# Kernel optimization log

Hardware: AMD Instinct MI355X
Metric: run time of the kernel (lower is better)

## Reference

```python
import jax, jax.numpy as jnp
import numpy as np

N_INPUT, N_QUBITS, N_LAYERS, N_CLASSES, BATCH = 64, 10, 6, 2, 16384


def _apply_1q(state, axis, m00, m01, m10, m11):
    # state: (B, 2,...,2) complex; axis is the tensor axis of the target wire.
    s = jnp.moveaxis(state, axis, -1)
    a0, a1 = s[..., 0], s[..., 1]
    b0 = m00 * a0 + m01 * a1
    b1 = m10 * a0 + m11 * a1
    return jnp.moveaxis(jnp.stack([b0, b1], axis=-1), -1, axis)


def _apply_cnot(state, control, target):
    # adjacent wires: target == control + 1 (tensor axes control+1, control+2)
    c_ax = control + 1
    s0 = jnp.take(state, 0, axis=c_ax)
    s1 = jnp.take(state, 1, axis=c_ax)
    s1 = jnp.flip(s1, axis=c_ax)  # target axis shifted down by 1 after take
    return jnp.stack([s0, s1], axis=c_ax)


def _simulate(angles, q_params):
    # angles: (B, n) per-sample RY embedding angles; q_params: (L*n*3,)
    B, n = angles.shape
    L = N_LAYERS
    w = q_params.reshape(L, n, 3)
    state = jnp.zeros((B,) + (2,) * n, dtype=jnp.complex64)
    state = state.at[(slice(None),) + (0,) * n].set(1.0)
    bshape = (B,) + (1,) * (n - 1)
    # data-encoding RY gates (per-sample angles)
    for i in range(n):
        th = angles[:, i].reshape(bshape) * 0.5
        c, s = jnp.cos(th), jnp.sin(th)
        state = _apply_1q(state, i + 1, c, -s, s, c)
    for l in range(L):
        for i in range(n):
            tx, ty, tz = w[l, i, 0] * 0.5, w[l, i, 1] * 0.5, w[l, i, 2] * 0.5
            cx, sx = jnp.cos(tx), jnp.sin(tx)
            state = _apply_1q(state, i + 1, cx, -1j * sx, -1j * sx, cx)  # RX
            cy, sy = jnp.cos(ty), jnp.sin(ty)
            state = _apply_1q(state, i + 1, cy, -sy, sy, cy)  # RY
            e = jnp.exp(-1j * tz)
            state = _apply_1q(state, i + 1, e, 0.0, 0.0, jnp.conj(e))  # RZ
        for i in range(n - 1):
            state = _apply_cnot(state, i, i + 1)
    probs = state.real ** 2 + state.imag ** 2  # (B, 2,...,2)
    other = lambda ax: tuple(a for a in range(1, n + 1) if a != ax)
    z = [jnp.sum(jnp.take(probs, 0, axis=i + 1), axis=tuple(range(1, n))) -
         jnp.sum(jnp.take(probs, 1, axis=i + 1), axis=tuple(range(1, n)))
         for i in range(n)]
    return jnp.stack(z, axis=-1)  # (B, n) <Z_i> expectations


def setup_inputs() -> dict:
    key = jax.random.key(0)
    ks = jax.random.split(key, 10)
    inp = {
        'x': jax.random.normal(ks[0], (BATCH, N_INPUT), dtype=jnp.float32),
        'W1': jax.random.normal(ks[1], (32, N_INPUT), dtype=jnp.float32) / np.sqrt(N_INPUT),
        'b1': jnp.zeros((32,), jnp.float32),
        'W2': jax.random.normal(ks[2], (N_QUBITS, 32), dtype=jnp.float32) / np.sqrt(32),
        'b2': jnp.zeros((N_QUBITS,), jnp.float32),
        'q_params': jax.random.normal(ks[3], (N_LAYERS * N_QUBITS * 3,), dtype=jnp.float32) * 0.01,
        'W3': jax.random.normal(ks[4], (16, N_QUBITS), dtype=jnp.float32) / np.sqrt(N_QUBITS),
        'b3': jnp.zeros((16,), jnp.float32),
        'W4': jax.random.normal(ks[5], (N_CLASSES, 16), dtype=jnp.float32) / 4.0,
        'b4': jnp.zeros((N_CLASSES,), jnp.float32),
    }
    return inp


def reference(x, W1, b1, W2, b2, q_params, W3, b3, W4, b4):
    h = jax.nn.relu(x @ W1.T + b1)
    angles = jnp.tanh(h @ W2.T + b2) * jnp.float32(np.pi)  # (B, n_qubits)
    z = _simulate(angles, q_params)                         # (B, n_qubits)
    h2 = jax.nn.relu(z @ W3.T + b3)
    return h2 @ W4.T + b4
```

## Files before the change

kernel.cpp:

```cpp
#include <hip/hip_runtime.h>
#include <hip/hip_fp16.h>

typedef unsigned int u32;
typedef __half2 h2;

__device__ __forceinline__ int   f2i(float x){ return __builtin_bit_cast(int, x); }
__device__ __forceinline__ float i2f(int x)  { return __builtin_bit_cast(float, x); }
__device__ __forceinline__ h2  b2h(u32 x){ return __builtin_bit_cast(h2, x); }
__device__ __forceinline__ u32 h2b(h2 x) { return __builtin_bit_cast(u32, x); }
__device__ __forceinline__ u32 rot16(u32 x){ return (x >> 16) | (x << 16); }

template<int PAT>
__device__ __forceinline__ float swzf(float x){
    return i2f(__builtin_amdgcn_ds_swizzle(f2i(x), PAT));
}
template<int PAT>
__device__ __forceinline__ u32 swzu(u32 x){
    return (u32)__builtin_amdgcn_ds_swizzle((int)x, PAT);
}
__device__ __forceinline__ float xor32f(float x){
    unsigned ux = __builtin_bit_cast(unsigned, x);
    auto r = __builtin_amdgcn_permlane32_swap(ux, ux, false, false);
    float a = __builtin_bit_cast(float, (unsigned)r[0]);
    float b = __builtin_bit_cast(float, (unsigned)r[1]);
    return (a + b) - x;
}
__device__ __forceinline__ float sum32(float x){
    unsigned ux = __builtin_bit_cast(unsigned, x);
    auto r = __builtin_amdgcn_permlane32_swap(ux, ux, false, false);
    float a = __builtin_bit_cast(float, (unsigned)r[0]);
    float b = __builtin_bit_cast(float, (unsigned)r[1]);
    return a + b;
}
__device__ __forceinline__ u32 sum32h(u32 x){
    auto r = __builtin_amdgcn_permlane32_swap(x, x, false, false);
    return h2b(__hadd2(b2h((u32)r[0]), b2h((u32)r[1])));
}
template<int B>
__device__ __forceinline__ float lx(float x){
    if constexpr      (B == 0) return swzf<0x041F>(x);
    else if constexpr (B == 1) return swzf<0x081F>(x);
    else if constexpr (B == 2) return swzf<0x101F>(x);
    else if constexpr (B == 3) return swzf<0x201F>(x);
    else if constexpr (B == 4) return swzf<0x401F>(x);
    else                       return xor32f(x);
}
template<int B>
__device__ __forceinline__ u32 lxu(u32 x){
    if constexpr      (B == 0) return swzu<0x041F>(x);
    else if constexpr (B == 1) return swzu<0x081F>(x);
    else if constexpr (B == 2) return swzu<0x101F>(x);
    else if constexpr (B == 3) return swzu<0x201F>(x);
    else                       return swzu<0x401F>(x);
}

__global__ void k_prep(const float* __restrict__ qp, float* __restrict__ ws)
{
    int t = threadIdx.x;
    if (t >= 60) return;
    int l = t / 10, q = t % 10;
    float tx = 0.5f * qp[t*3 + 0];
    float ty = 0.5f * qp[t*3 + 1];
    float tz = 0.5f * qp[t*3 + 2];
    float cx = cosf(tx), sx = sinf(tx);
    float cy = cosf(ty), sy = sinf(ty);
    float cz, sz;
    if (l == 5) { cz = 1.0f; sz = 0.0f; }
    else        { cz = cosf(tz); sz = sinf(tz); }
    float m00r =  cy*cx, m00i =  sy*sx;
    float m01r = -sy*cx, m01i = -cy*sx;
    float m10r =  sy*cx, m10i = -cy*sx;
    float m11r =  cy*cx, m11i = -sy*sx;
    float U[8];
    U[0] = m00r*cz + m00i*sz;  U[1] = m00i*cz - m00r*sz;
    U[2] = m01r*cz + m01i*sz;  U[3] = m01i*cz - m01r*sz;
    U[4] = m10r*cz - m10i*sz;  U[5] = m10i*cz + m10r*sz;
    U[6] = m11r*cz - m11i*sz;  U[7] = m11i*cz + m11r*sz;
    #pragma unroll
    for (int j = 0; j < 8; j++) ws[t*8 + j] = U[j];

    if (l >= 1) {
        u32* W = reinterpret_cast<u32*>(ws) + 480 + (l-1)*80 + q*8;
        auto pk2 = [](float a, float b){
            return __builtin_bit_cast(u32, __floats2half2_rn(a, b));
        };
        if (q == 9) {
            W[0] = pk2(U[0],  U[6]);
            W[1] = pk2(-U[1], -U[7]);
            W[2] = pk2(U[2],  U[4]);
            W[3] = pk2(-U[3], -U[5]);
            W[4] = pk2(U[1],  U[7]);
            W[5] = pk2(U[3],  U[5]);
            W[6] = 0; W[7] = 0;
        } else {
            #pragma unroll
            for (int j = 0; j < 8; j++) W[j] = pk2(U[j], U[j]);
        }
    }
}


__device__ __forceinline__ void chainH(u32 (&a)[8], int baddr, bool lpar)
{
    #pragma unroll
    for (int k = 0; k < 4; k++) {
        u32 t0 = a[2*k], t1 = a[2*k+1];
        a[2*k]   = lpar ? t1 : t0;
        a[2*k+1] = lpar ? t0 : t1;
    }
    auto BP = [&](u32 v){ return (u32)__builtin_amdgcn_ds_bpermute(baddr, (int)v); };
    u32 n0 = BP(a[0]);
    u32 n1 = BP(a[3]);
    u32 n2 = BP(a[6]);
    u32 n3 = BP(a[5]);
    u32 n4 = rot16(BP(a[4]));
    u32 n5 = rot16(BP(a[7]));
    u32 n6 = rot16(BP(a[2]));
    u32 n7 = rot16(BP(a[1]));
    a[0]=n0; a[1]=n1; a[2]=n2; a[3]=n3; a[4]=n4; a[5]=n5; a[6]=n6; a[7]=n7;
}

template<int B>
__device__ __forceinline__ void lane_gateH(u32 (&pr)[8], u32 (&pi)[8],
                                           const u32* __restrict__ W, int lane)
{
    u32 w0=W[0], w1=W[1], w2=W[2], w3=W[3], w4=W[4], w5=W[5], w6=W[6], w7=W[7];
    bool hi = (lane >> B) & 1;
    h2 Msr = b2h(hi ? w6 : w0), Msi = b2h(hi ? w7 : w1);
    h2 Mor = b2h(hi ? w4 : w2), Moi = b2h(hi ? w5 : w3);
    h2 nMsi = __hneg2(Msi), nMoi = __hneg2(Moi);
    #pragma unroll
    for (int k = 0; k < 8; k++){
        h2 a  = b2h(pr[k]), b = b2h(pi[k]);
        h2 oa = b2h(lxu<B>(pr[k]));
        h2 ob = b2h(lxu<B>(pi[k]));
        h2 nr = __hfma2(Msr, a, __hfma2(nMsi, b, __hfma2(Mor, oa, __hmul2(nMoi, ob))));
        h2 ni = __hfma2(Msr, b, __hfma2(Msi, a, __hfma2(Mor, ob, __hmul2(Moi, oa))));
        pr[k] = h2b(nr); pi[k] = h2b(ni);
    }
}

__device__ __forceinline__ void lane_gateS5H(u32 (&pr)[8], u32 (&pi)[8],
                                             const u32* __restrict__ W, int lane)
{
    u32 w0=W[0], w1=W[1], w2=W[2], w3=W[3], w4=W[4], w5=W[5], w6=W[6], w7=W[7];
    bool hi = (lane >> 5) & 1;
    h2 Msr = b2h(hi ? w6 : w0), Msi = b2h(hi ? w7 : w1);
    h2 Mor = b2h(hi ? w4 : w2), Moi = b2h(hi ? w5 : w3);
    h2 dsr = __hsub2(Msr, Mor), dsi = __hsub2(Msi, Moi);
    h2 ndsi = __hneg2(dsi), nMoi = __hneg2(Moi);
    #pragma unroll
    for (int k = 0; k < 8; k++){
        h2 a  = b2h(pr[k]), b = b2h(pi[k]);
        h2 Sr = b2h(sum32h(pr[k]));
        h2 Si = b2h(sum32h(pi[k]));
        h2 nr = __hfma2(dsr, a, __hfma2(ndsi, b, __hfma2(Mor, Sr, __hmul2(nMoi, Si))));
        h2 ni = __hfma2(dsr, b, __hfma2(dsi, a, __hfma2(Mor, Si, __hmul2(Moi, Sr))));
        pr[k] = h2b(nr); pi[k] = h2b(ni);
    }
}

template<int M2>
__device__ __forceinline__ void reg_gateH(u32 (&pr)[8], u32 (&pi)[8],
                                          const u32* __restrict__ W)
{
    h2 U00r=b2h(W[0]), U00i=b2h(W[1]), U01r=b2h(W[2]), U01i=b2h(W[3]);
    h2 U10r=b2h(W[4]), U10i=b2h(W[5]), U11r=b2h(W[6]), U11i=b2h(W[7]);
    h2 n00i=__hneg2(U00i), n01i=__hneg2(U01i), n10i=__hneg2(U10i), n11i=__hneg2(U11i);
    #pragma unroll
    for (int k = 0; k < 8; k++) if (!(k & M2)) {
        const int k2 = k | M2;
        h2 A0r=b2h(pr[k]), A0i=b2h(pi[k]), A1r=b2h(pr[k2]), A1i=b2h(pi[k2]);
        pr[k]  = h2b(__hfma2(U00r,A0r, __hfma2(n00i,A0i, __hfma2(U01r,A1r, __hmul2(n01i,A1i)))));
        pi[k]  = h2b(__hfma2(U00r,A0i, __hfma2(U00i,A0r, __hfma2(U01r,A1i, __hmul2(U01i,A1r)))));
        pr[k2] = h2b(__hfma2(U10r,A0r, __hfma2(n10i,A0i, __hfma2(U11r,A1r, __hmul2(n11i,A1i)))));
        pi[k2] = h2b(__hfma2(U10r,A0i, __hfma2(U10i,A0r, __hfma2(U11r,A1i, __hmul2(U11i,A1r)))));
    }
}

__device__ __forceinline__ void q9_gateH(u32 (&pr)[8], u32 (&pi)[8],
                                         const u32* __restrict__ W)
{
    h2 Ar=b2h(W[0]), Br=b2h(W[1]), Cr=b2h(W[2]), Dr=b2h(W[3]);
    h2 Ai2=b2h(W[4]), Ci2=b2h(W[5]);
    #pragma unroll
    for (int k = 0; k < 8; k++){
        h2 a  = b2h(pr[k]),        b  = b2h(pi[k]);
        h2 as = b2h(rot16(pr[k])), bs = b2h(rot16(pi[k]));
        h2 nr = __hfma2(Ar,  a, __hfma2(Br, b, __hfma2(Cr,  as, __hmul2(Dr, bs))));
        h2 ni = __hfma2(Ai2, a, __hfma2(Ar, b, __hfma2(Ci2, as, __hmul2(Cr, bs))));
        pr[k] = h2b(nr); pi[k] = h2b(ni);
    }
}

template<int B>
__device__ __forceinline__ float st_signed(float v, int lane){
    float t = lx<B>(v);
    return ((lane >> B) & 1) ? (t - v) : (v - t);
}
template<int B>
__device__ __forceinline__ float st_plain(float v){
    if constexpr (B == 5) return sum32(v);
    else return v + lx<B>(v);
}
template<int I>
__device__ __forceinline__ float z_mixed(float S, int lane){
    float v = st_signed<0>(S, lane);
    if constexpr (I >= 1) v = st_signed<1>(v, lane); else v = st_plain<1>(v);
    if constexpr (I >= 2) v = st_signed<2>(v, lane); else v = st_plain<2>(v);
    if constexpr (I >= 3) v = st_signed<3>(v, lane); else v = st_plain<3>(v);
    if constexpr (I >= 4) v = st_signed<4>(v, lane); else v = st_plain<4>(v);
    if constexpr (I >= 5) v = st_signed<5>(v, lane); else v = st_plain<5>(v);
    return v;
}

__global__ __launch_bounds__(256)
__attribute__((amdgpu_waves_per_eu(5, 8)))
void k_qsim(
        const float* __restrict__ x,
        const float* __restrict__ W1, const float* __restrict__ b1,
        const float* __restrict__ W2, const float* __restrict__ b2,
        const float* __restrict__ ws,
        const float* __restrict__ W3, const float* __restrict__ b3,
        const float* __restrict__ W4, const float* __restrict__ b4,
        float* __restrict__ out)
{
    const int lane = threadIdx.x & 63;
    int wid = (blockIdx.x * 256 + threadIdx.x) >> 6;
    const int s = __builtin_amdgcn_readfirstlane(wid);

    float cv[10], sv[10];
    {
        const float* xr  = x + s * 64;
        const int j = lane & 31;
        const float* w1r = W1 + j * 64;
        float a = b1[j];
        #pragma unroll
        for (int k = 0; k < 64; k += 4) {
            float4 xv = *reinterpret_cast<const float4*>(xr + k);
            float4 wv = *reinterpret_cast<const float4*>(w1r + k);
            a = fmaf(wv.x, xv.x, a);
            a = fmaf(wv.y, xv.y, a);
            a = fmaf(wv.z, xv.z, a);
            a = fmaf(wv.w, xv.w, a);
        }
        float h = fmaxf(a, 0.0f);

        float tsel = 0.0f;
        #pragma unroll
        for (int i = 0; i < 10; i++) {
            float t = W2[i*32 + j] * h;
            t = st_plain<4>(t);  t = st_plain<3>(t);  t = st_plain<2>(t);
            t = st_plain<1>(t);  t = st_plain<0>(t);
            t += b2[i];
            if (lane == i) tsel = t;
        }
        float ang = tanhf(tsel) * 1.5707963267948966f;
        float sA, cA;
        __sincosf(ang, &sA, &cA);
        #pragma unroll
        for (int q = 0; q < 10; q++) {
            cv[q] = i2f(__builtin_amdgcn_readlane(f2i(cA), q));
            sv[q] = i2f(__builtin_amdgcn_readlane(f2i(sA), q));
        }
    }

    u32 pr[8], pi[8];

    {
        const float* U0 = ws;
        float Lr, Li;
        {
            float v0r = U0[0]*cv[0] + U0[2]*sv[0], v0i = U0[1]*cv[0] + U0[3]*sv[0];
            float v1r = U0[4]*cv[0] + U0[6]*sv[0], v1i = U0[5]*cv[0] + U0[7]*sv[0];
            bool b = lane & 1;
            Lr = b ? v1r : v0r;  Li = b ? v1i : v0i;
        }
        #pragma unroll
        for (int q = 1; q < 6; q++) {
            const float* U = U0 + q*8;
            float v0r = U[0]*cv[q] + U[2]*sv[q], v0i = U[1]*cv[q] + U[3]*sv[q];
            float v1r = U[4]*cv[q] + U[6]*sv[q], v1i = U[5]*cv[q] + U[7]*sv[q];
            bool b = (lane >> q) & 1;
            float fr = b ? v1r : v0r, fi = b ? v1i : v0i;
            float nr = Lr*fr - Li*fi;
            float ni = Lr*fi + Li*fr;
            Lr = nr; Li = ni;
        }
        float vr[4][2], vi[4][2];
        #pragma unroll
        for (int q = 6; q < 10; q++) {
            const float* U = U0 + q*8;
            vr[q-6][0] = U[0]*cv[q] + U[2]*sv[q];  vi[q-6][0] = U[1]*cv[q] + U[3]*sv[q];
            vr[q-6][1] = U[4]*cv[q] + U[6]*sv[q];  vi[q-6][1] = U[5]*cv[q] + U[7]*sv[q];
        }
        float t67r[4], t67i[4], t89r[4], t89i[4];
        #pragma unroll
        for (int m = 0; m < 4; m++) {
            int b0 = m & 1, b1i = (m >> 1) & 1;
            t67r[m] = vr[0][b0]*vr[1][b1i] - vi[0][b0]*vi[1][b1i];
            t67i[m] = vr[0][b0]*vi[1][b1i] + vi[0][b0]*vr[1][b1i];
            t89r[m] = vr[2][b0]*vr[3][b1i] - vi[2][b0]*vi[3][b1i];
            t89i[m] = vr[2][b0]*vi[3][b1i] + vi[2][b0]*vr[3][b1i];
        }
        #pragma unroll
        for (int p = 0; p < 8; p++) {
            const int lo = p & 3, h0 = p >> 2, h1 = h0 + 2;
            float prr0 = t67r[lo]*t89r[h0] - t67i[lo]*t89i[h0];
            float pii0 = t67r[lo]*t89i[h0] + t67i[lo]*t89r[h0];
            float re0 = Lr*prr0 - Li*pii0, im0 = Lr*pii0 + Li*prr0;
            float prr1 = t67r[lo]*t89r[h1] - t67i[lo]*t89i[h1];
            float pii1 = t67r[lo]*t89i[h1] + t67i[lo]*t89r[h1];
            float re1 = Lr*prr1 - Li*pii1, im1 = Lr*pii1 + Li*prr1;
            pr[p] = __builtin_bit_cast(u32, __floats2half2_rn(re0, re1));
            pi[p] = __builtin_bit_cast(u32, __floats2half2_rn(im0, im1));
        }
    }

    const int  baddr = ((lane ^ (lane << 1)) & 63) << 2;
    const bool lpar  = __builtin_popcount(lane & 63) & 1;
    const u32* WH = reinterpret_cast<const u32*>(ws) + 480;

    #pragma unroll 1
    for (int l = 0; l < 5; ++l) {
        chainH(pr, baddr, lpar);
        chainH(pi, baddr, lpar);
        const u32* Ub = WH + l * 80;
        lane_gateH<0>(pr, pi, Ub +  0, lane);
        lane_gateH<1>(pr, pi, Ub +  8, lane);
        lane_gateH<2>(pr, pi, Ub + 16, lane);
        lane_gateH<3>(pr, pi, Ub + 24, lane);
        lane_gateH<4>(pr, pi, Ub + 32, lane);
        lane_gateS5H (pr, pi, Ub + 40, lane);
        reg_gateH<1> (pr, pi, Ub + 48);
        reg_gateH<2> (pr, pi, Ub + 56);
        reg_gateH<4> (pr, pi, Ub + 64);
        q9_gateH     (pr, pi, Ub + 72);
    }

    float P[16];
    #pragma unroll
    for (int p = 0; p < 8; p++) {
        h2 a = b2h(pr[p]), b = b2h(pi[p]);
        float arl = __low2float(a),  ail = __low2float(b);
        float arh = __high2float(a), aih = __high2float(b);
        P[p]     = arl*arl + ail*ail;
        P[p + 8] = arh*arh + aih*aih;
    }
    float u[8], d[8];
    #pragma unroll
    for (int k = 0; k < 8; k++) { u[k] = P[2*k] + P[2*k+1]; d[k] = P[2*k] - P[2*k+1]; }
    float S  = ((u[0]+u[1]) + (u[2]+u[3])) + ((u[4]+u[5]) + (u[6]+u[7]));
    float T0 = ((d[0]+d[1]) + (d[2]+d[3])) + ((d[4]+d[5]) + (d[6]+d[7]));
    float e0 = d[0]-d[1], e1 = d[2]-d[3], e2 = d[4]-d[5], e3 = d[6]-d[7];
    float T1 = (e0+e1) + (e2+e3);
    float f0 = e0-e1, f1 = e2-e3;
    float T2 = f0 + f1;
    float T3 = f0 - f1;

    float z[10];
    z[0] = z_mixed<0>(S, lane);
    z[1] = z_mixed<1>(S, lane);
    z[2] = z_mixed<2>(S, lane);
    z[3] = z_mixed<3>(S, lane);
    z[4] = z_mixed<4>(S, lane);
    z[5] = z_mixed<5>(S, lane);
    z[6] = z_mixed<5>(T0, lane);
    z[7] = z_mixed<5>(T1, lane);
    z[8] = z_mixed<5>(T2, lane);
    z[9] = z_mixed<5>(T3, lane);

    float acc0 = b4[0], acc1 = b4[1];
    #pragma unroll
    for (int j2 = 0; j2 < 16; j2++) {
        float a = b3[j2];
        #pragma unroll
        for (int q = 0; q < 10; q++) a = fmaf(W3[j2*10 + q], z[q], a);
        a = fmaxf(a, 0.0f);
        acc0 = fmaf(W4[j2],      a, acc0);
        acc1 = fmaf(W4[16 + j2], a, acc1);
    }
    if (lane == 0) {
        reinterpret_cast<float2*>(out)[s] = make_float2(acc0, acc1);
    }
}

extern "C" void kernel_launch(void* const* d_in, const int* in_sizes, int n_in,
                              void* d_out, int out_size, void* d_ws, size_t ws_size,
                              hipStream_t stream)
{
    (void)in_sizes; (void)n_in; (void)out_size; (void)ws_size;
    const float* x  = (const float*)d_in[0];
    const float* W1 = (const float*)d_in[1];
    const float* b1 = (const float*)d_in[2];
    const float* W2 = (const float*)d_in[3];
    const float* b2 = (const float*)d_in[4];
    const float* qp = (const float*)d_in[5];
    const float* W3 = (const float*)d_in[6];
    const float* b3 = (const float*)d_in[7];
    const float* W4 = (const float*)d_in[8];
    const float* b4 = (const float*)d_in[9];
    float* ws  = (float*)d_ws;
    float* out = (float*)d_out;

    k_prep<<<1, 64, 0, stream>>>(qp, ws);
    k_qsim<<<4096, 256, 0, stream>>>(x, W1, b1, W2, b2, ws, W3, b3, W4, b4, out);
}
```

Measured before the change: 163.1 us.

## Simulate two samples per wavefront to amortize gate setup and raise ILP

```diff
diff --git a/kernel.cpp b/kernel.cpp
--- a/kernel.cpp
+++ b/kernel.cpp
@@ -121,8 +121,9 @@
 }
 
 template<int B>
-__device__ __forceinline__ void lane_gateH(u32 (&pr)[8], u32 (&pi)[8],
-                                           const u32* __restrict__ W, int lane)
+__device__ __forceinline__ void lane_gateH2(u32 (&prA)[8], u32 (&piA)[8],
+                                            u32 (&prB)[8], u32 (&piB)[8],
+                                            const u32* __restrict__ W, int lane)
 {
     u32 w0=W[0], w1=W[1], w2=W[2], w3=W[3], w4=W[4], w5=W[5], w6=W[6], w7=W[7];
     bool hi = (lane >> B) & 1;
@@ -131,17 +132,24 @@
     h2 nMsi = __hneg2(Msi), nMoi = __hneg2(Moi);
     #pragma unroll
     for (int k = 0; k < 8; k++){
-        h2 a  = b2h(pr[k]), b = b2h(pi[k]);
-        h2 oa = b2h(lxu<B>(pr[k]));
-        h2 ob = b2h(lxu<B>(pi[k]));
-        h2 nr = __hfma2(Msr, a, __hfma2(nMsi, b, __hfma2(Mor, oa, __hmul2(nMoi, ob))));
-        h2 ni = __hfma2(Msr, b, __hfma2(Msi, a, __hfma2(Mor, ob, __hmul2(Moi, oa))));
-        pr[k] = h2b(nr); pi[k] = h2b(ni);
-    }
-}
-
-__device__ __forceinline__ void lane_gateS5H(u32 (&pr)[8], u32 (&pi)[8],
-                                             const u32* __restrict__ W, int lane)
+        h2 aA  = b2h(prA[k]), bA = b2h(piA[k]);
+        h2 aB  = b2h(prB[k]), bB = b2h(piB[k]);
+        h2 oaA = b2h(lxu<B>(prA[k]));
+        h2 obA = b2h(lxu<B>(piA[k]));
+        h2 oaB = b2h(lxu<B>(prB[k]));
+        h2 obB = b2h(lxu<B>(piB[k]));
+        h2 nrA = __hfma2(Msr, aA, __hfma2(nMsi, bA, __hfma2(Mor, oaA, __hmul2(nMoi, obA))));
+        h2 niA = __hfma2(Msr, bA, __hfma2(Msi, aA, __hfma2(Mor, obA, __hmul2(Moi, oaA))));
+        h2 nrB = __hfma2(Msr, aB, __hfma2(nMsi, bB, __hfma2(Mor, oaB, __hmul2(nMoi, obB))));
+        h2 niB = __hfma2(Msr, bB, __hfma2(Msi, aB, __hfma2(Mor, obB, __hmul2(Moi, oaB))));
+        prA[k] = h2b(nrA); piA[k] = h2b(niA);
+        prB[k] = h2b(nrB); piB[k] = h2b(niB);
+    }
+}
+
+__device__ __forceinline__ void lane_gateS5H2(u32 (&prA)[8], u32 (&piA)[8],
+                                              u32 (&prB)[8], u32 (&piB)[8],
+                                              const u32* __restrict__ W, int lane)
 {
     u32 w0=W[0], w1=W[1], w2=W[2], w3=W[3], w4=W[4], w5=W[5], w6=W[6], w7=W[7];
     bool hi = (lane >> 5) & 1;
@@ -151,18 +159,25 @@
     h2 ndsi = __hneg2(dsi), nMoi = __hneg2(Moi);
     #pragma unroll
     for (int k = 0; k < 8; k++){
-        h2 a  = b2h(pr[k]), b = b2h(pi[k]);
-        h2 Sr = b2h(sum32h(pr[k]));
-        h2 Si = b2h(sum32h(pi[k]));
-        h2 nr = __hfma2(dsr, a, __hfma2(ndsi, b, __hfma2(Mor, Sr, __hmul2(nMoi, Si))));
-        h2 ni = __hfma2(dsr, b, __hfma2(dsi, a, __hfma2(Mor, Si, __hmul2(Moi, Sr))));
-        pr[k] = h2b(nr); pi[k] = h2b(ni);
+        h2 aA = b2h(prA[k]), bA = b2h(piA[k]);
+        h2 aB = b2h(prB[k]), bB = b2h(piB[k]);
+        h2 SrA = b2h(sum32h(prA[k]));
+        h2 SiA = b2h(sum32h(piA[k]));
+        h2 SrB = b2h(sum32h(prB[k]));
+        h2 SiB = b2h(sum32h(piB[k]));
+        h2 nrA = __hfma2(dsr, aA, __hfma2(ndsi, bA, __hfma2(Mor, SrA, __hmul2(nMoi, SiA))));
+        h2 niA = __hfma2(dsr, bA, __hfma2(dsi, aA, __hfma2(Mor, SiA, __hmul2(Moi, SrA))));
+        h2 nrB = __hfma2(dsr, aB, __hfma2(ndsi, bB, __hfma2(Mor, SrB, __hmul2(nMoi, SiB))));
+        h2 niB = __hfma2(dsr, bB, __hfma2(dsi, aB, __hfma2(Mor, SiB, __hmul2(Moi, SrB))));
+        prA[k] = h2b(nrA); piA[k] = h2b(niA);
+        prB[k] = h2b(nrB); piB[k] = h2b(niB);
     }
 }
 
 template<int M2>
-__device__ __forceinline__ void reg_gateH(u32 (&pr)[8], u32 (&pi)[8],
-                                          const u32* __restrict__ W)
+__device__ __forceinline__ void reg_gateH2(u32 (&prA)[8], u32 (&piA)[8],
+                                           u32 (&prB)[8], u32 (&piB)[8],
+                                           const u32* __restrict__ W)
 {
     h2 U00r=b2h(W[0]), U00i=b2h(W[1]), U01r=b2h(W[2]), U01i=b2h(W[3]);
     h2 U10r=b2h(W[4]), U10i=b2h(W[5]), U11r=b2h(W[6]), U11i=b2h(W[7]);
@@ -170,26 +185,91 @@
     #pragma unroll
     for (int k = 0; k < 8; k++) if (!(k & M2)) {
         const int k2 = k | M2;
-        h2 A0r=b2h(pr[k]), A0i=b2h(pi[k]), A1r=b2h(pr[k2]), A1i=b2h(pi[k2]);
-        pr[k]  = h2b(__hfma2(U00r,A0r, __hfma2(n00i,A0i, __hfma2(U01r,A1r, __hmul2(n01i,A1i)))));
-        pi[k]  = h2b(__hfma2(U00r,A0i, __hfma2(U00i,A0r, __hfma2(U01r,A1i, __hmul2(U01i,A1r)))));
-        pr[k2] = h2b(__hfma2(U10r,A0r, __hfma2(n10i,A0i, __hfma2(U11r,A1r, __hmul2(n11i,A1i)))));
-        pi[k2] = h2b(__hfma2(U10r,A0i, __hfma2(U10i,A0r, __hfma2(U11r,A1i, __hmul2(U11i,A1r)))));
-    }
-}
-
-__device__ __forceinline__ void q9_gateH(u32 (&pr)[8], u32 (&pi)[8],
-                                         const u32* __restrict__ W)
+        {
+            h2 A0r=b2h(prA[k]), A0i=b2h(piA[k]), A1r=b2h(prA[k2]), A1i=b2h(piA[k2]);
+            prA[k]  = h2b(__hfma2(U00r,A0r, __hfma2(n00i,A0i, __hfma2(U01r,A1r, __hmul2(n01i,A1i)))));
+            piA[k]  = h2b(__hfma2(U00r,A0i, __hfma2(U00i,A0r, __hfma2(U01r,A1i, __hmul2(U01i,A1r)))));
+            prA[k2] = h2b(__hfma2(U10r,A0r, __hfma2(n10i,A0i, __hfma2(U11r,A1r, __hmul2(n11i,A1i)))));
+            piA[k2] = h2b(__hfma2(U10r,A0i, __hfma2(U10i,A0r, __hfma2(U11r,A1i, __hmul2(U11i,A1r)))));
+        }
+        {
+            h2 A0r=b2h(prB[k]), A0i=b2h(piB[k]), A1r=b2h(prB[k2]), A1i=b2h(piB[k2]);
+            prB[k]  = h2b(__hfma2(U00r,A0r, __hfma2(n00i,A0i, __hfma2(U01r,A1r, __hmul2(n01i,A1i)))));
+            piB[k]  = h2b(__hfma2(U00r,A0i, __hfma2(U00i,A0r, __hfma2(U01r,A1i, __hmul2(U01i,A1r)))));
+            prB[k2] = h2b(__hfma2(U10r,A0r, __hfma2(n10i,A0i, __hfma2(U11r,A1r, __hmul2(n11i,A1i)))));
+            piB[k2] = h2b(__hfma2(U10r,A0i, __hfma2(U10i,A0r, __hfma2(U11r,A1i, __hmul2(U11i,A1r)))));
+        }
+    }
+}
+
+__device__ __forceinline__ void q9_gateH2(u32 (&prA)[8], u32 (&piA)[8],
+                                          u32 (&prB)[8], u32 (&piB)[8],
+                                          const u32* __restrict__ W)
 {
     h2 Ar=b2h(W[0]), Br=b2h(W[1]), Cr=b2h(W[2]), Dr=b2h(W[3]);
     h2 Ai2=b2h(W[4]), Ci2=b2h(W[5]);
     #pragma unroll
     for (int k = 0; k < 8; k++){
-        h2 a  = b2h(pr[k]),        b  = b2h(pi[k]);
-        h2 as = b2h(rot16(pr[k])), bs = b2h(rot16(pi[k]));
-        h2 nr = __hfma2(Ar,  a, __hfma2(Br, b, __hfma2(Cr,  as, __hmul2(Dr, bs))));
-        h2 ni = __hfma2(Ai2, a, __hfma2(Ar, b, __hfma2(Ci2, as, __hmul2(Cr, bs))));
-        pr[k] = h2b(nr); pi[k] = h2b(ni);
+        h2 aA  = b2h(prA[k]),        bA  = b2h(piA[k]);
+        h2 asA = b2h(rot16(prA[k])), bsA = b2h(rot16(piA[k]));
+        h2 aB  = b2h(prB[k]),        bB  = b2h(piB[k]);
+        h2 asB = b2h(rot16(prB[k])), bsB = b2h(rot16(piB[k]));
+        prA[k] = h2b(__hfma2(Ar,  aA, __hfma2(Br, bA, __hfma2(Cr,  asA, __hmul2(Dr, bsA)))));
+        piA[k] = h2b(__hfma2(Ai2, aA, __hfma2(Ar, bA, __hfma2(Ci2, asA, __hmul2(Cr, bsA)))));
+        prB[k] = h2b(__hfma2(Ar,  aB, __hfma2(Br, bB, __hfma2(Cr,  asB, __hmul2(Dr, bsB)))));
+        piB[k] = h2b(__hfma2(Ai2, aB, __hfma2(Ar, bB, __hfma2(Ci2, asB, __hmul2(Cr, bsB)))));
+    }
+}
+
+__device__ __forceinline__ void init_stateH(u32 (&pr)[8], u32 (&pi)[8],
+                                            const float (&cv)[10], const float (&sv)[10],
+                                            const float* __restrict__ U0, int lane)
+{
+    float Lr, Li;
+    {
+        float v0r = U0[0]*cv[0] + U0[2]*sv[0], v0i = U0[1]*cv[0] + U0[3]*sv[0];
+        float v1r = U0[4]*cv[0] + U0[6]*sv[0], v1i = U0[5]*cv[0] + U0[7]*sv[0];
+        bool b = lane & 1;
+        Lr = b ? v1r : v0r;  Li = b ? v1i : v0i;
+    }
+    #pragma unroll
+    for (int q = 1; q < 6; q++) {
+        const float* U = U0 + q*8;
+        float v0r = U[0]*cv[q] + U[2]*sv[q], v0i = U[1]*cv[q] + U[3]*sv[q];
+        float v1r = U[4]*cv[q] + U[6]*sv[q], v1i = U[5]*cv[q] + U[7]*sv[q];
+        bool b = (lane >> q) & 1;
+        float fr = b ? v1r : v0r, fi = b ? v1i : v0i;
+        float nr = Lr*fr - Li*fi;
+        float ni = Lr*fi + Li*fr;
+        Lr = nr; Li = ni;
+    }
+    float vr[4][2], vi[4][2];
+    #pragma unroll
+    for (int q = 6; q < 10; q++) {
+        const float* U = U0 + q*8;
+        vr[q-6][0] = U[0]*cv[q] + U[2]*sv[q];  vi[q-6][0] = U[1]*cv[q] + U[3]*sv[q];
+        vr[q-6][1] = U[4]*cv[q] + U[6]*sv[q];  vi[q-6][1] = U[5]*cv[q] + U[7]*sv[q];
+    }
+    float t67r[4], t67i[4], t89r[4], t89i[4];
+    #pragma unroll
+    for (int m = 0; m < 4; m++) {
+        int b0 = m & 1, b1i = (m >> 1) & 1;
+        t67r[m] = vr[0][b0]*vr[1][b1i] - vi[0][b0]*vi[1][b1i];
+        t67i[m] = vr[0][b0]*vi[1][b1i] + vi[0][b0]*vr[1][b1i];
+        t89r[m] = vr[2][b0]*vr[3][b1i] - vi[2][b0]*vi[3][b1i];
+        t89i[m] = vr[2][b0]*vi[3][b1i] + vi[2][b0]*vr[3][b1i];
+    }
+    #pragma unroll
+    for (int p = 0; p < 8; p++) {
+        const int lo = p & 3, h0 = p >> 2, h1 = h0 + 2;
+        float prr0 = t67r[lo]*t89r[h0] - t67i[lo]*t89i[h0];
+        float pii0 = t67r[lo]*t89i[h0] + t67i[lo]*t89r[h0];
+        float re0 = Lr*prr0 - Li*pii0, im0 = Lr*pii0 + Li*prr0;
+        float prr1 = t67r[lo]*t89r[h1] - t67i[lo]*t89i[h1];
+        float pii1 = t67r[lo]*t89i[h1] + t67i[lo]*t89r[h1];
+        float re1 = Lr*prr1 - Li*pii1, im1 = Lr*pii1 + Li*prr1;
+        pr[p] = __builtin_bit_cast(u32, __floats2half2_rn(re0, re1));
+        pi[p] = __builtin_bit_cast(u32, __floats2half2_rn(im0, im1));
     }
 }
 
@@ -214,8 +294,42 @@
     return v;
 }
 
+__device__ __forceinline__ void readoutH(const u32 (&pr)[8], const u32 (&pi)[8],
+                                         int lane, float (&z)[10])
+{
+    float P[16];
+    #pragma unroll
+    for (int p = 0; p < 8; p++) {
+        h2 a = b2h(pr[p]), b = b2h(pi[p]);
+        float arl = __low2float(a),  ail = __low2float(b);
+        float arh = __high2float(a), aih = __high2float(b);
+        P[p]     = arl*arl + ail*ail;
+        P[p + 8] = arh*arh + aih*aih;
+    }
+    float u[8], d[8];
+    #pragma unroll
+    for (int k = 0; k < 8; k++) { u[k] = P[2*k] + P[2*k+1]; d[k] = P[2*k] - P[2*k+1]; }
+    float S  = ((u[0]+u[1]) + (u[2]+u[3])) + ((u[4]+u[5]) + (u[6]+u[7]));
+    float T0 = ((d[0]+d[1]) + (d[2]+d[3])) + ((d[4]+d[5]) + (d[6]+d[7]));
+    float e0 = d[0]-d[1], e1 = d[2]-d[3], e2 = d[4]-d[5], e3 = d[6]-d[7];
+    float T1 = (e0+e1) + (e2+e3);
+    float f0 = e0-e1, f1 = e2-e3;
+    float T2 = f0 + f1;
+    float T3 = f0 - f1;
+    z[0] = z_mixed<0>(S, lane);
+    z[1] = z_mixed<1>(S, lane);
+    z[2] = z_mixed<2>(S, lane);
+    z[3] = z_mixed<3>(S, lane);
+    z[4] = z_mixed<4>(S, lane);
+    z[5] = z_mixed<5>(S, lane);
+    z[6] = z_mixed<5>(T0, lane);
+    z[7] = z_mixed<5>(T1, lane);
+    z[8] = z_mixed<5>(T2, lane);
+    z[9] = z_mixed<5>(T3, lane);
+}
+
 __global__ __launch_bounds__(256)
-__attribute__((amdgpu_waves_per_eu(5, 8)))
+__attribute__((amdgpu_waves_per_eu(6, 8)))
 void k_qsim(
         const float* __restrict__ x,
         const float* __restrict__ W1, const float* __restrict__ b1,
@@ -226,13 +340,13 @@
         float* __restrict__ out)
 {
     const int lane = threadIdx.x & 63;
-    int wid = (blockIdx.x * 256 + threadIdx.x) >> 6;
-    const int s = __builtin_amdgcn_readfirstlane(wid);
-
-    float cv[10], sv[10];
+    int wid0 = (blockIdx.x * 256 + threadIdx.x) >> 6;
+    const int wid = __builtin_amdgcn_readfirstlane(wid0);
+
+    float cA, sA;
     {
-        const float* xr  = x + s * 64;
         const int j = lane & 31;
+        const float* xr  = x + (2*wid + (lane >> 5)) * 64;
         const float* w1r = W1 + j * 64;
         float a = b1[j];
         #pragma unroll
@@ -253,68 +367,27 @@
             t = st_plain<4>(t);  t = st_plain<3>(t);  t = st_plain<2>(t);
             t = st_plain<1>(t);  t = st_plain<0>(t);
             t += b2[i];
-            if (lane == i) tsel = t;
+            if (j == i) tsel = t;
         }
         float ang = tanhf(tsel) * 1.5707963267948966f;
-        float sA, cA;
         __sincosf(ang, &sA, &cA);
+    }
+
+    u32 prA[8], piA[8], prB[8], piB[8];
+    {
+        float cv[10], sv[10];
         #pragma unroll
         for (int q = 0; q < 10; q++) {
             cv[q] = i2f(__builtin_amdgcn_readlane(f2i(cA), q));
             sv[q] = i2f(__builtin_amdgcn_readlane(f2i(sA), q));
         }
-    }
-
-    u32 pr[8], pi[8];
-
-    {
-        const float* U0 = ws;
-        float Lr, Li;
-        {
-            float v0r = U0[0]*cv[0] + U0[2]*sv[0], v0i = U0[1]*cv[0] + U0[3]*sv[0];
-            float v1r = U0[4]*cv[0] + U0[6]*sv[0], v1i = U0[5]*cv[0] + U0[7]*sv[0];
-            bool b = lane & 1;
-            Lr = b ? v1r : v0r;  Li = b ? v1i : v0i;
-        }
+        init_stateH(prA, piA, cv, sv, ws, lane);
         #pragma unroll
-        for (int q = 1; q < 6; q++) {
-            const float* U = U0 + q*8;
-            float v0r = U[0]*cv[q] + U[2]*sv[q], v0i = U[1]*cv[q] + U[3]*sv[q];
-            float v1r = U[4]*cv[q] + U[6]*sv[q], v1i = U[5]*cv[q] + U[7]*sv[q];
-            bool b = (lane >> q) & 1;
-            float fr = b ? v1r : v0r, fi = b ? v1i : v0i;
-            float nr = Lr*fr - Li*fi;
-            float ni = Lr*fi + Li*fr;
-            Lr = nr; Li = ni;
-        }
-        float vr[4][2], vi[4][2];
-        #pragma unroll
-        for (int q = 6; q < 10; q++) {
-            const float* U = U0 + q*8;
-            vr[q-6][0] = U[0]*cv[q] + U[2]*sv[q];  vi[q-6][0] = U[1]*cv[q] + U[3]*sv[q];
-            vr[q-6][1] = U[4]*cv[q] + U[6]*sv[q];  vi[q-6][1] = U[5]*cv[q] + U[7]*sv[q];
-        }
-        float t67r[4], t67i[4], t89r[4], t89i[4];
-        #pragma unroll
-        for (int m = 0; m < 4; m++) {
-            int b0 = m & 1, b1i = (m >> 1) & 1;
-            t67r[m] = vr[0][b0]*vr[1][b1i] - vi[0][b0]*vi[1][b1i];
-            t67i[m] = vr[0][b0]*vi[1][b1i] + vi[0][b0]*vr[1][b1i];
-            t89r[m] = vr[2][b0]*vr[3][b1i] - vi[2][b0]*vi[3][b1i];
-            t89i[m] = vr[2][b0]*vi[3][b1i] + vi[2][b0]*vr[3][b1i];
-        }
-        #pragma unroll
-        for (int p = 0; p < 8; p++) {
-            const int lo = p & 3, h0 = p >> 2, h1 = h0 + 2;
-            float prr0 = t67r[lo]*t89r[h0] - t67i[lo]*t89i[h0];
-            float pii0 = t67r[lo]*t89i[h0] + t67i[lo]*t89r[h0];
-            float re0 = Lr*prr0 - Li*pii0, im0 = Lr*pii0 + Li*prr0;
-            float prr1 = t67r[lo]*t89r[h1] - t67i[lo]*t89i[h1];
-            float pii1 = t67r[lo]*t89i[h1] + t67i[lo]*t89r[h1];
-            float re1 = Lr*prr1 - Li*pii1, im1 = Lr*pii1 + Li*prr1;
-            pr[p] = __builtin_bit_cast(u32, __floats2half2_rn(re0, re1));
-            pi[p] = __builtin_bit_cast(u32, __floats2half2_rn(im0, im1));
-        }
+        for (int q = 0; q < 10; q++) {
+            cv[q] = i2f(__builtin_amdgcn_readlane(f2i(cA), 32 + q));
+            sv[q] = i2f(__builtin_amdgcn_readlane(f2i(sA), 32 + q));
+        }
+        init_stateH(prB, piB, cv, sv, ws, lane);
     }
 
     const int  baddr = ((lane ^ (lane << 1)) & 63) << 2;
@@ -323,65 +396,48 @@
 
     #pragma unroll 1
     for (int l = 0; l < 5; ++l) {
-        chainH(pr, baddr, lpar);
-        chainH(pi, baddr, lpar);
+        chainH(prA, baddr, lpar);
+        chainH(piA, baddr, lpar);
+        chainH(prB, baddr, lpar);
+        chainH(piB, baddr, lpar);
         const u32* Ub = WH + l * 80;
-        lane_gateH<0>(pr, pi, Ub +  0, lane);
-        lane_gateH<1>(pr, pi, Ub +  8, lane);
-        lane_gateH<2>(pr, pi, Ub + 16, lane);
-        lane_gateH<3>(pr, pi, Ub + 24, lane);
-        lane_gateH<4>(pr, pi, Ub + 32, lane);
-        lane_gateS5H (pr, pi, Ub + 40, lane);
-        reg_gateH<1> (pr, pi, Ub + 48);
-        reg_gateH<2> (pr, pi, Ub + 56);
-        reg_gateH<4> (pr, pi, Ub + 64);
-        q9_gateH     (pr, pi, Ub + 72);
-    }
-
-    float P[16];
-    #pragma unroll
-    for (int p = 0; p < 8; p++) {
-        h2 a = b2h(pr[p]), b = b2h(pi[p]);
-        float arl = __low2float(a),  ail = __low2float(b);
-        float arh = __high2float(a), aih = __high2float(b);
-        P[p]     = arl*arl + ail*ail;
-        P[p + 8] = arh*arh + aih*aih;
-    }
-    float u[8], d[8];
-    #pragma unroll
-    for (int k = 0; k < 8; k++) { u[k] = P[2*k] + P[2*k+1]; d[k] = P[2*k] - P[2*k+1]; }
-    float S  = ((u[0]+u[1]) + (u[2]+u[3])) + ((u[4]+u[5]) + (u[6]+u[7]));
-    float T0 = ((d[0]+d[1]) + (d[2]+d[3])) + ((d[4]+d[5]) + (d[6]+d[7]));
-    float e0 = d[0]-d[1], e1 = d[2]-d[3], e2 = d[4]-d[5], e3 = d[6]-d[7];
-    float T1 = (e0+e1) + (e2+e3);
-    float f0 = e0-e1, f1 = e2-e3;
-    float T2 = f0 + f1;
-    float T3 = f0 - f1;
-
-    float z[10];
-    z[0] = z_mixed<0>(S, lane);
-    z[1] = z_mixed<1>(S, lane);
-    z[2] = z_mixed<2>(S, lane);
-    z[3] = z_mixed<3>(S, lane);
-    z[4] = z_mixed<4>(S, lane);
-    z[5] = z_mixed<5>(S, lane);
-    z[6] = z_mixed<5>(T0, lane);
-    z[7] = z_mixed<5>(T1, lane);
-    z[8] = z_mixed<5>(T2, lane);
-    z[9] = z_mixed<5>(T3, lane);
-
-    float acc0 = b4[0], acc1 = b4[1];
+        lane_gateH2<0>(prA, piA, prB, piB, Ub +  0, lane);
+        lane_gateH2<1>(prA, piA, prB, piB, Ub +  8, lane);
+        lane_gateH2<2>(prA, piA, prB, piB, Ub + 16, lane);
+        lane_gateH2<3>(prA, piA, prB, piB, Ub + 24, lane);
+        lane_gateH2<4>(prA, piA, prB, piB, Ub + 32, lane);
+        lane_gateS5H2 (prA, piA, prB, piB, Ub + 40, lane);
+        reg_gateH2<1> (prA, piA, prB, piB, Ub + 48);
+        reg_gateH2<2> (prA, piA, prB, piB, Ub + 56);
+        reg_gateH2<4> (prA, piA, prB, piB, Ub + 64);
+        q9_gateH2     (prA, piA, prB, piB, Ub + 72);
+    }
+
+    float zA[10], zB[10];
+    readoutH(prA, piA, lane, zA);
+    readoutH(prB, piB, lane, zB);
+
+    float a0A = b4[0], a1A = b4[1], a0B = b4[0], a1B = b4[1];
     #pragma unroll
     for (int j2 = 0; j2 < 16; j2++) {
-        float a = b3[j2];
+        float aA = b3[j2], aB = b3[j2];
         #pragma unroll
-        for (int q = 0; q < 10; q++) a = fmaf(W3[j2*10 + q], z[q], a);
-        a = fmaxf(a, 0.0f);
-        acc0 = fmaf(W4[j2],      a, acc0);
-        acc1 = fmaf(W4[16 + j2], a, acc1);
+        for (int q = 0; q < 10; q++) {
+            float w = W3[j2*10 + q];
+            aA = fmaf(w, zA[q], aA);
+            aB = fmaf(w, zB[q], aB);
+        }
+        aA = fmaxf(aA, 0.0f);
+        aB = fmaxf(aB, 0.0f);
+        float w40 = W4[j2], w41 = W4[16 + j2];
+        a0A = fmaf(w40, aA, a0A);
+        a1A = fmaf(w41, aA, a1A);
+        a0B = fmaf(w40, aB, a0B);
+        a1B = fmaf(w41, aB, a1B);
     }
     if (lane == 0) {
-        reinterpret_cast<float2*>(out)[s] = make_float2(acc0, acc1);
+        float4 o; o.x = a0A; o.y = a1A; o.z = a0B; o.w = a1B;
+        reinterpret_cast<float4*>(out)[wid] = o;
     }
 }
 
@@ -404,5 +460,5 @@
     float* out = (float*)d_out;
 
     k_prep<<<1, 64, 0, stream>>>(qp, ws);
-    k_qsim<<<4096, 256, 0, stream>>>(x, W1, b1, W2, b2, ws, W3, b3, W4, b4, out);
-}
+    k_qsim<<<2048, 256, 0, stream>>>(x, W1, b1, W2, b2, ws, W3, b3, W4, b4, out);
+}
```

Result: slower. 168.7 us (+3.4%).
